# Kernel tuning notes

Measured on AMD Instinct MI355X. Metric: run time of the kernel, lower is better.

Reference implementation:

```python
import jax, jax.numpy as jnp
import numpy as np

C0 = 0.5 * np.sqrt(1.0 / np.pi)
C1 = np.sqrt(3.0 / (4 * np.pi))
C2 = 0.5 * np.sqrt(15.0 / (4 * np.pi))
C20 = 0.5 * np.sqrt(5.0 / (16 * np.pi))
C22 = 0.5 * np.sqrt(15.0 / (16 * np.pi))


def sh_basis(d):
    # d: [N,3] unit directions -> [N,9] (degree 2, matches torch code order)
    x, y, z = d[:, 0], d[:, 1], d[:, 2]
    return jnp.stack([
        C0 * jnp.ones_like(x),
        C1 * y, C1 * z, C1 * x,
        C2 * x * y, C2 * y * z,
        C20 * (3 * z * z - 1),
        C2 * x * z,
        C22 * (x * x - y * y),
    ], axis=-1)


def trilinear_sample(voxels, pts_norm):
    # voxels: [R,R,R,F] indexed (z,y,x); pts_norm: [N,3] in [-1,1] (x,y,z)
    # Matches F.grid_sample(align_corners=True, padding_mode='border').
    R = voxels.shape[0]
    c = jnp.clip((pts_norm + 1.0) * 0.5 * (R - 1), 0.0, R - 1)  # border clamp
    c0 = jnp.floor(c)
    f = c - c0                          # [N,3] fractional weights (fx,fy,fz)
    i0 = c0.astype(jnp.int32)
    i1 = jnp.minimum(i0 + 1, R - 1)
    x0, y0, z0 = i0[:, 0], i0[:, 1], i0[:, 2]
    x1, y1, z1 = i1[:, 0], i1[:, 1], i1[:, 2]
    fx, fy, fz = f[:, 0:1], f[:, 1:2], f[:, 2:3]
    g = lambda zi, yi, xi: voxels[zi, yi, xi]  # gather -> [N,F]
    c00 = g(z0, y0, x0) * (1 - fx) + g(z0, y0, x1) * fx
    c01 = g(z0, y1, x0) * (1 - fx) + g(z0, y1, x1) * fx
    c10 = g(z1, y0, x0) * (1 - fx) + g(z1, y0, x1) * fx
    c11 = g(z1, y1, x0) * (1 - fx) + g(z1, y1, x1) * fx
    c0_ = c00 * (1 - fy) + c01 * fy
    c1_ = c10 * (1 - fy) + c11 * fy
    return c0_ * (1 - fz) + c1_ * fz


def setup_inputs() -> dict:
    key = jax.random.key(0)
    k1, k2 = jax.random.split(key)
    N, R, F = 2_000_000, 192, 28
    points = jax.random.normal(k1, (N, 3), dtype=jnp.float32)
    voxels = jax.random.normal(k2, (R, R, R, F), dtype=jnp.float32) * 0.1
    return {"points": points, "voxels": voxels}


def reference(points, voxels):
    N = points.shape[0]
    sh_dim = 9
    pts_norm = points / 4.0
    feats = trilinear_sample(voxels, pts_norm)         # [N, 28]
    density = feats[:, 0]
    sh = feats[:, 1:].reshape(N, 3, sh_dim)            # [N,3,9]
    d = points / jnp.linalg.norm(points, axis=-1, keepdims=True)
    basis = sh_basis(d)[:, None, :]                    # [N,1,9]
    rgb = jax.nn.sigmoid(jnp.sum(sh * basis, axis=-1))  # [N,3]
    sigma = jax.nn.softplus(density)[:, None]           # [N,1]
    return rgb, sigma
```

## Files before the change

### kernel.cpp

```cpp
#include <hip/hip_runtime.h>
#include <math.h>

#define RDIM 192
#define FDIM 28
#define PTS_PER_BLOCK 32

#define SH_C0  0.28209479177387814f
#define SH_C1  0.4886025119029199f
#define SH_C2  0.5462742152960396f
#define SH_C20 0.15769578262626154f
#define SH_C22 0.2731371076480198f

__global__ __launch_bounds__(256)
void plenoxel_fwd(const float* __restrict__ points,
                  const float* __restrict__ voxels,
                  float* __restrict__ out_rgb,
                  float* __restrict__ out_sigma,
                  int N)
{
    __shared__ float feats[PTS_PER_BLOCK][FDIM];

    const int tid   = threadIdx.x;
    const int group = tid >> 3;
    const int f     = tid & 7;
    const int p     = blockIdx.x * PTS_PER_BLOCK + group;

    if (p < N && f < 7) {
        float px = points[3 * p + 0];
        float py = points[3 * p + 1];
        float pz = points[3 * p + 2];

        const float A = (RDIM - 1) / 8.0f;
        const float B = (RDIM - 1) * 0.5f;
        const float RM1 = (float)(RDIM - 1);
        float cx = fminf(fmaxf(px * A + B, 0.0f), RM1);
        float cy = fminf(fmaxf(py * A + B, 0.0f), RM1);
        float cz = fminf(fmaxf(pz * A + B, 0.0f), RM1);

        float cx0 = floorf(cx), cy0 = floorf(cy), cz0 = floorf(cz);
        float fx = cx - cx0, fy = cy - cy0, fz = cz - cz0;
        int x0 = (int)cx0, y0 = (int)cy0, z0 = (int)cz0;
        int x1 = min(x0 + 1, RDIM - 1);
        int y1 = min(y0 + 1, RDIM - 1);
        int z1 = min(z0 + 1, RDIM - 1);

        float gx = 1.0f - fx, gy = 1.0f - fy, gz = 1.0f - fz;

        float w000 = gz * gy * gx;
        float w001 = gz * gy * fx;
        float w010 = gz * fy * gx;
        float w011 = gz * fy * fx;
        float w100 = fz * gy * gx;
        float w101 = fz * gy * fx;
        float w110 = fz * fy * gx;
        float w111 = fz * fy * fx;

        int b000 = ((z0 * RDIM + y0) * RDIM + x0) * FDIM;
        int b001 = ((z0 * RDIM + y0) * RDIM + x1) * FDIM;
        int b010 = ((z0 * RDIM + y1) * RDIM + x0) * FDIM;
        int b011 = ((z0 * RDIM + y1) * RDIM + x1) * FDIM;
        int b100 = ((z1 * RDIM + y0) * RDIM + x0) * FDIM;
        int b101 = ((z1 * RDIM + y0) * RDIM + x1) * FDIM;
        int b110 = ((z1 * RDIM + y1) * RDIM + x0) * FDIM;
        int b111 = ((z1 * RDIM + y1) * RDIM + x1) * FDIM;

        const float4* __restrict__ src = (const float4*)voxels;

        float4 v0 = src[(b000 >> 2) + f];
        float4 v1 = src[(b001 >> 2) + f];
        float4 v2 = src[(b010 >> 2) + f];
        float4 v3 = src[(b011 >> 2) + f];
        float4 v4 = src[(b100 >> 2) + f];
        float4 v5 = src[(b101 >> 2) + f];
        float4 v6 = src[(b110 >> 2) + f];
        float4 v7 = src[(b111 >> 2) + f];

        float4 acc;
        acc.x = w000 * v0.x + w001 * v1.x + w010 * v2.x + w011 * v3.x
              + w100 * v4.x + w101 * v5.x + w110 * v6.x + w111 * v7.x;
        acc.y = w000 * v0.y + w001 * v1.y + w010 * v2.y + w011 * v3.y
              + w100 * v4.y + w101 * v5.y + w110 * v6.y + w111 * v7.y;
        acc.z = w000 * v0.z + w001 * v1.z + w010 * v2.z + w011 * v3.z
              + w100 * v4.z + w101 * v5.z + w110 * v6.z + w111 * v7.z;
        acc.w = w000 * v0.w + w001 * v1.w + w010 * v2.w + w011 * v3.w
              + w100 * v4.w + w101 * v5.w + w110 * v6.w + w111 * v7.w;

        *(float4*)&feats[group][4 * f] = acc;
    }

    __syncthreads();

    if (tid < PTS_PER_BLOCK) {
        int p2 = blockIdx.x * PTS_PER_BLOCK + tid;
        if (p2 < N) {
            float px = points[3 * p2 + 0];
            float py = points[3 * p2 + 1];
            float pz = points[3 * p2 + 2];

            float inv = rsqrtf(px * px + py * py + pz * pz);
            float dx = px * inv, dy = py * inv, dz = pz * inv;

            float basis[9];
            basis[0] = SH_C0;
            basis[1] = SH_C1 * dy;
            basis[2] = SH_C1 * dz;
            basis[3] = SH_C1 * dx;
            basis[4] = SH_C2 * dx * dy;
            basis[5] = SH_C2 * dy * dz;
            basis[6] = SH_C20 * (3.0f * dz * dz - 1.0f);
            basis[7] = SH_C2 * dx * dz;
            basis[8] = SH_C22 * (dx * dx - dy * dy);

#pragma unroll
            for (int c = 0; c < 3; ++c) {
                float s = 0.0f;
#pragma unroll
                for (int j = 0; j < 9; ++j) {
                    s += feats[tid][1 + 9 * c + j] * basis[j];
                }
                out_rgb[3 * p2 + c] = 1.0f / (1.0f + expf(-s));
            }

            float x = feats[tid][0];
            out_sigma[p2] = fmaxf(x, 0.0f) + log1pf(expf(-fabsf(x)));
        }
    }
}

extern "C" void kernel_launch(void* const* d_in, const int* in_sizes, int n_in,
                              void* d_out, int out_size, void* d_ws, size_t ws_size,
                              hipStream_t stream) {
    const float* points = (const float*)d_in[0];
    const float* voxels = (const float*)d_in[1];
    int N = in_sizes[0] / 3;

    float* out_rgb = (float*)d_out;
    float* out_sigma = out_rgb + (size_t)3 * N;

    int blocks = (N + PTS_PER_BLOCK - 1) / PTS_PER_BLOCK;
    plenoxel_fwd<<<blocks, 256, 0, stream>>>(points, voxels, out_rgb, out_sigma, N);
}
```

Baseline: 354.3 us.

## Bucket-sort points by voxel block before trilinear gather for locality

```diff
diff --git a/kernel.cpp b/kernel.cpp
--- a/kernel.cpp
+++ b/kernel.cpp
@@ -4,6 +4,10 @@
 #define RDIM 192
 #define FDIM 28
 #define PTS_PER_BLOCK 32
+
+#define BSHIFT 3
+#define BDIM   (RDIM >> BSHIFT)
+#define NBUCKET (BDIM * BDIM * BDIM)
 
 #define SH_C0  0.28209479177387814f
 #define SH_C1  0.4886025119029199f
@@ -11,8 +15,89 @@
 #define SH_C20 0.15769578262626154f
 #define SH_C22 0.2731371076480198f
 
-__global__ __launch_bounds__(256)
-void plenoxel_fwd(const float* __restrict__ points,
+__device__ __forceinline__ void cell_of(float px, float py, float pz,
+                                        int& x0, int& y0, int& z0) {
+    const float A = (RDIM - 1) / 8.0f;
+    const float B = (RDIM - 1) * 0.5f;
+    const float RM1 = (float)(RDIM - 1);
+    float cx = fminf(fmaxf(px * A + B, 0.0f), RM1);
+    float cy = fminf(fmaxf(py * A + B, 0.0f), RM1);
+    float cz = fminf(fmaxf(pz * A + B, 0.0f), RM1);
+    x0 = (int)floorf(cx);
+    y0 = (int)floorf(cy);
+    z0 = (int)floorf(cz);
+}
+
+__device__ __forceinline__ int bucket_of(int x0, int y0, int z0) {
+    return ((z0 >> BSHIFT) * BDIM + (y0 >> BSHIFT)) * BDIM + (x0 >> BSHIFT);
+}
+
+__global__ __launch_bounds__(256)
+void zero_hist(int* __restrict__ hist) {
+    int i = blockIdx.x * 256 + threadIdx.x;
+    if (i < NBUCKET) hist[i] = 0;
+}
+
+__global__ __launch_bounds__(256)
+void hist_kernel(const float* __restrict__ points, int* __restrict__ hist, int N) {
+    int i = blockIdx.x * 256 + threadIdx.x;
+    if (i >= N) return;
+    float px = points[3 * i + 0];
+    float py = points[3 * i + 1];
+    float pz = points[3 * i + 2];
+    int x0, y0, z0;
+    cell_of(px, py, pz, x0, y0, z0);
+    atomicAdd(&hist[bucket_of(x0, y0, z0)], 1);
+}
+
+#define SCAN_T 1024
+#define SCAN_V 14
+__global__ __launch_bounds__(SCAN_T)
+void scan_kernel(const int* __restrict__ hist, int* __restrict__ offs) {
+    __shared__ int lds[SCAN_T];
+    int t = threadIdx.x;
+    int base = t * SCAN_V;
+    int v[SCAN_V];
+    int s = 0;
+#pragma unroll
+    for (int k = 0; k < SCAN_V; ++k) {
+        int idx = base + k;
+        v[k] = (idx < NBUCKET) ? hist[idx] : 0;
+        s += v[k];
+    }
+    lds[t] = s;
+    __syncthreads();
+    for (int off = 1; off < SCAN_T; off <<= 1) {
+        int add = (t >= off) ? lds[t - off] : 0;
+        __syncthreads();
+        lds[t] += add;
+        __syncthreads();
+    }
+    int excl = (t == 0) ? 0 : lds[t - 1];
+#pragma unroll
+    for (int k = 0; k < SCAN_V; ++k) {
+        int idx = base + k;
+        if (idx < NBUCKET) offs[idx] = excl;
+        excl += v[k];
+    }
+}
+
+__global__ __launch_bounds__(256)
+void scatter_kernel(const float* __restrict__ points, int* __restrict__ offs,
+                    float4* __restrict__ sorted, int N) {
+    int i = blockIdx.x * 256 + threadIdx.x;
+    if (i >= N) return;
+    float px = points[3 * i + 0];
+    float py = points[3 * i + 1];
+    float pz = points[3 * i + 2];
+    int x0, y0, z0;
+    cell_of(px, py, pz, x0, y0, z0);
+    int pos = atomicAdd(&offs[bucket_of(x0, y0, z0)], 1);
+    sorted[pos] = make_float4(px, py, pz, __int_as_float(i));
+}
+
+__global__ __launch_bounds__(256)
+void plenoxel_fwd(const float4* __restrict__ sorted,
                   const float* __restrict__ voxels,
                   float* __restrict__ out_rgb,
                   float* __restrict__ out_sigma,
@@ -26,20 +111,18 @@
     const int p     = blockIdx.x * PTS_PER_BLOCK + group;
 
     if (p < N && f < 7) {
-        float px = points[3 * p + 0];
-        float py = points[3 * p + 1];
-        float pz = points[3 * p + 2];
-
+        float4 pt = sorted[p];
+        float px = pt.x, py = pt.y, pz = pt.z;
+
+        int x0, y0, z0;
+        cell_of(px, py, pz, x0, y0, z0);
         const float A = (RDIM - 1) / 8.0f;
         const float B = (RDIM - 1) * 0.5f;
         const float RM1 = (float)(RDIM - 1);
         float cx = fminf(fmaxf(px * A + B, 0.0f), RM1);
         float cy = fminf(fmaxf(py * A + B, 0.0f), RM1);
         float cz = fminf(fmaxf(pz * A + B, 0.0f), RM1);
-
-        float cx0 = floorf(cx), cy0 = floorf(cy), cz0 = floorf(cz);
-        float fx = cx - cx0, fy = cy - cy0, fz = cz - cz0;
-        int x0 = (int)cx0, y0 = (int)cy0, z0 = (int)cz0;
+        float fx = cx - (float)x0, fy = cy - (float)y0, fz = cz - (float)z0;
         int x1 = min(x0 + 1, RDIM - 1);
         int y1 = min(y0 + 1, RDIM - 1);
         int z1 = min(z0 + 1, RDIM - 1);
@@ -93,9 +176,9 @@
     if (tid < PTS_PER_BLOCK) {
         int p2 = blockIdx.x * PTS_PER_BLOCK + tid;
         if (p2 < N) {
-            float px = points[3 * p2 + 0];
-            float py = points[3 * p2 + 1];
-            float pz = points[3 * p2 + 2];
+            float4 pt = sorted[p2];
+            float px = pt.x, py = pt.y, pz = pt.z;
+            int oi = __float_as_int(pt.w);
 
             float inv = rsqrtf(px * px + py * py + pz * pz);
             float dx = px * inv, dy = py * inv, dz = pz * inv;
@@ -118,11 +201,11 @@
                 for (int j = 0; j < 9; ++j) {
                     s += feats[tid][1 + 9 * c + j] * basis[j];
                 }
-                out_rgb[3 * p2 + c] = 1.0f / (1.0f + expf(-s));
+                out_rgb[3 * oi + c] = 1.0f / (1.0f + expf(-s));
             }
 
             float x = feats[tid][0];
-            out_sigma[p2] = fmaxf(x, 0.0f) + log1pf(expf(-fabsf(x)));
+            out_sigma[oi] = fmaxf(x, 0.0f) + log1pf(expf(-fabsf(x)));
         }
     }
 }
@@ -137,6 +220,18 @@
     float* out_rgb = (float*)d_out;
     float* out_sigma = out_rgb + (size_t)3 * N;
 
-    int blocks = (N + PTS_PER_BLOCK - 1) / PTS_PER_BLOCK;
-    plenoxel_fwd<<<blocks, 256, 0, stream>>>(points, voxels, out_rgb, out_sigma, N);
-}
+    char* ws = (char*)d_ws;
+    float4* sorted = (float4*)ws;
+    int* hist = (int*)(ws + (size_t)N * 16);
+    int* offs = hist + NBUCKET;
+
+    int pblocks = (N + 255) / 256;
+
+    zero_hist<<<(NBUCKET + 255) / 256, 256, 0, stream>>>(hist);
+    hist_kernel<<<pblocks, 256, 0, stream>>>(points, hist, N);
+    scan_kernel<<<1, SCAN_T, 0, stream>>>(hist, offs);
+    scatter_kernel<<<pblocks, 256, 0, stream>>>(points, offs, sorted, N);
+
+    int gblocks = (N + PTS_PER_BLOCK - 1) / PTS_PER_BLOCK;
+    plenoxel_fwd<<<gblocks, 256, 0, stream>>>(sorted, voxels, out_rgb, out_sigma, N);
+}
```

Result: slower. 823.3 us (+132.3%).

## Process two points per thread group to double in-flight gathers

Applied to the files above, without the earlier changes.

```diff
diff --git a/kernel.cpp b/kernel.cpp
--- a/kernel.cpp
+++ b/kernel.cpp
@@ -3,7 +3,7 @@
 
 #define RDIM 192
 #define FDIM 28
-#define PTS_PER_BLOCK 32
+#define PPB 64
 
 #define SH_C0  0.28209479177387814f
 #define SH_C1  0.4886025119029199f
@@ -18,84 +18,101 @@
                   float* __restrict__ out_sigma,
                   int N)
 {
-    __shared__ float feats[PTS_PER_BLOCK][FDIM];
+    __shared__ float feats[PPB][FDIM];
+    __shared__ float4 plds[PPB];
 
     const int tid   = threadIdx.x;
     const int group = tid >> 3;
     const int f     = tid & 7;
-    const int p     = blockIdx.x * PTS_PER_BLOCK + group;
+    const int pbase = blockIdx.x * PPB;
+    const float4* __restrict__ src = (const float4*)voxels;
 
-    if (p < N && f < 7) {
-        float px = points[3 * p + 0];
-        float py = points[3 * p + 1];
-        float pz = points[3 * p + 2];
+    const float A   = (RDIM - 1) / 8.0f;
+    const float B   = (RDIM - 1) * 0.5f;
+    const float RM1 = (float)(RDIM - 1);
 
-        const float A = (RDIM - 1) / 8.0f;
-        const float B = (RDIM - 1) * 0.5f;
-        const float RM1 = (float)(RDIM - 1);
-        float cx = fminf(fmaxf(px * A + B, 0.0f), RM1);
-        float cy = fminf(fmaxf(py * A + B, 0.0f), RM1);
-        float cz = fminf(fmaxf(pz * A + B, 0.0f), RM1);
+    if (f < 7) {
+#define POINT_SETUP(h, PIDX)                                                  \
+        const int p##h  = (PIDX);                                             \
+        const int cp##h = min(p##h, N - 1);                                   \
+        const float px##h = points[3 * cp##h + 0];                            \
+        const float py##h = points[3 * cp##h + 1];                            \
+        const float pz##h = points[3 * cp##h + 2];                            \
+        if (f == 0) plds[group + 32 * h] =                                    \
+            make_float4(px##h, py##h, pz##h, 0.0f);                           \
+        float cx##h = fminf(fmaxf(px##h * A + B, 0.0f), RM1);                 \
+        float cy##h = fminf(fmaxf(py##h * A + B, 0.0f), RM1);                 \
+        float cz##h = fminf(fmaxf(pz##h * A + B, 0.0f), RM1);                 \
+        float fcx##h = floorf(cx##h), fcy##h = floorf(cy##h),                 \
+              fcz##h = floorf(cz##h);                                         \
+        float fx##h = cx##h - fcx##h, fy##h = cy##h - fcy##h,                 \
+              fz##h = cz##h - fcz##h;                                         \
+        int x0##h = (int)fcx##h, y0##h = (int)fcy##h, z0##h = (int)fcz##h;    \
+        int x1##h = min(x0##h + 1, RDIM - 1);                                 \
+        int y1##h = min(y0##h + 1, RDIM - 1);                                 \
+        int z1##h = min(z0##h + 1, RDIM - 1);                                 \
+        float gx##h = 1.0f - fx##h, gy##h = 1.0f - fy##h,                     \
+              gz##h = 1.0f - fz##h;                                           \
+        float w##h##0 = gz##h * gy##h * gx##h;                                \
+        float w##h##1 = gz##h * gy##h * fx##h;                                \
+        float w##h##2 = gz##h * fy##h * gx##h;                                \
+        float w##h##3 = gz##h * fy##h * fx##h;                                \
+        float w##h##4 = fz##h * gy##h * gx##h;                                \
+        float w##h##5 = fz##h * gy##h * fx##h;                                \
+        float w##h##6 = fz##h * fy##h * gx##h;                                \
+        float w##h##7 = fz##h * fy##h * fx##h;                                \
+        int a##h##0 = ((((z0##h * RDIM + y0##h) * RDIM + x0##h) * FDIM) >> 2) + f; \
+        int a##h##1 = ((((z0##h * RDIM + y0##h) * RDIM + x1##h) * FDIM) >> 2) + f; \
+        int a##h##2 = ((((z0##h * RDIM + y1##h) * RDIM + x0##h) * FDIM) >> 2) + f; \
+        int a##h##3 = ((((z0##h * RDIM + y1##h) * RDIM + x1##h) * FDIM) >> 2) + f; \
+        int a##h##4 = ((((z1##h * RDIM + y0##h) * RDIM + x0##h) * FDIM) >> 2) + f; \
+        int a##h##5 = ((((z1##h * RDIM + y0##h) * RDIM + x1##h) * FDIM) >> 2) + f; \
+        int a##h##6 = ((((z1##h * RDIM + y1##h) * RDIM + x0##h) * FDIM) >> 2) + f; \
+        int a##h##7 = ((((z1##h * RDIM + y1##h) * RDIM + x1##h) * FDIM) >> 2) + f;
 
-        float cx0 = floorf(cx), cy0 = floorf(cy), cz0 = floorf(cz);
-        float fx = cx - cx0, fy = cy - cy0, fz = cz - cz0;
-        int x0 = (int)cx0, y0 = (int)cy0, z0 = (int)cz0;
-        int x1 = min(x0 + 1, RDIM - 1);
-        int y1 = min(y0 + 1, RDIM - 1);
-        int z1 = min(z0 + 1, RDIM - 1);
+        POINT_SETUP(0, pbase + group)
+        POINT_SETUP(1, pbase + group + 32)
+#undef POINT_SETUP
 
-        float gx = 1.0f - fx, gy = 1.0f - fy, gz = 1.0f - fz;
+        float4 v00 = src[a00]; float4 v01 = src[a01];
+        float4 v02 = src[a02]; float4 v03 = src[a03];
+        float4 v04 = src[a04]; float4 v05 = src[a05];
+        float4 v06 = src[a06]; float4 v07 = src[a07];
+        float4 v10 = src[a10]; float4 v11 = src[a11];
+        float4 v12 = src[a12]; float4 v13 = src[a13];
+        float4 v14 = src[a14]; float4 v15 = src[a15];
+        float4 v16 = src[a16]; float4 v17 = src[a17];
 
-        float w000 = gz * gy * gx;
-        float w001 = gz * gy * fx;
-        float w010 = gz * fy * gx;
-        float w011 = gz * fy * fx;
-        float w100 = fz * gy * gx;
-        float w101 = fz * gy * fx;
-        float w110 = fz * fy * gx;
-        float w111 = fz * fy * fx;
+#define ACC_STORE(h, V0, V1, V2, V3, V4, V5, V6, V7, ROW)                     \
+        {                                                                     \
+            float4 acc;                                                       \
+            acc.x = w##h##0 * V0.x + w##h##1 * V1.x + w##h##2 * V2.x          \
+                  + w##h##3 * V3.x + w##h##4 * V4.x + w##h##5 * V5.x          \
+                  + w##h##6 * V6.x + w##h##7 * V7.x;                          \
+            acc.y = w##h##0 * V0.y + w##h##1 * V1.y + w##h##2 * V2.y          \
+                  + w##h##3 * V3.y + w##h##4 * V4.y + w##h##5 * V5.y          \
+                  + w##h##6 * V6.y + w##h##7 * V7.y;                          \
+            acc.z = w##h##0 * V0.z + w##h##1 * V1.z + w##h##2 * V2.z          \
+                  + w##h##3 * V3.z + w##h##4 * V4.z + w##h##5 * V5.z          \
+                  + w##h##6 * V6.z + w##h##7 * V7.z;                          \
+            acc.w = w##h##0 * V0.w + w##h##1 * V1.w + w##h##2 * V2.w          \
+                  + w##h##3 * V3.w + w##h##4 * V4.w + w##h##5 * V5.w          \
+                  + w##h##6 * V6.w + w##h##7 * V7.w;                          \
+            *(float4*)&feats[ROW][4 * f] = acc;                               \
+        }
 
-        int b000 = ((z0 * RDIM + y0) * RDIM + x0) * FDIM;
-        int b001 = ((z0 * RDIM + y0) * RDIM + x1) * FDIM;
-        int b010 = ((z0 * RDIM + y1) * RDIM + x0) * FDIM;
-        int b011 = ((z0 * RDIM + y1) * RDIM + x1) * FDIM;
-        int b100 = ((z1 * RDIM + y0) * RDIM + x0) * FDIM;
-        int b101 = ((z1 * RDIM + y0) * RDIM + x1) * FDIM;
-        int b110 = ((z1 * RDIM + y1) * RDIM + x0) * FDIM;
-        int b111 = ((z1 * RDIM + y1) * RDIM + x1) * FDIM;
-
-        const float4* __restrict__ src = (const float4*)voxels;
-
-        float4 v0 = src[(b000 >> 2) + f];
-        float4 v1 = src[(b001 >> 2) + f];
-        float4 v2 = src[(b010 >> 2) + f];
-        float4 v3 = src[(b011 >> 2) + f];
-        float4 v4 = src[(b100 >> 2) + f];
-        float4 v5 = src[(b101 >> 2) + f];
-        float4 v6 = src[(b110 >> 2) + f];
-        float4 v7 = src[(b111 >> 2) + f];
-
-        float4 acc;
-        acc.x = w000 * v0.x + w001 * v1.x + w010 * v2.x + w011 * v3.x
-              + w100 * v4.x + w101 * v5.x + w110 * v6.x + w111 * v7.x;
-        acc.y = w000 * v0.y + w001 * v1.y + w010 * v2.y + w011 * v3.y
-              + w100 * v4.y + w101 * v5.y + w110 * v6.y + w111 * v7.y;
-        acc.z = w000 * v0.z + w001 * v1.z + w010 * v2.z + w011 * v3.z
-              + w100 * v4.z + w101 * v5.z + w110 * v6.z + w111 * v7.z;
-        acc.w = w000 * v0.w + w001 * v1.w + w010 * v2.w + w011 * v3.w
-              + w100 * v4.w + w101 * v5.w + w110 * v6.w + w111 * v7.w;
-
-        *(float4*)&feats[group][4 * f] = acc;
+        ACC_STORE(0, v00, v01, v02, v03, v04, v05, v06, v07, group)
+        ACC_STORE(1, v10, v11, v12, v13, v14, v15, v16, v17, group + 32)
+#undef ACC_STORE
     }
 
     __syncthreads();
 
-    if (tid < PTS_PER_BLOCK) {
-        int p2 = blockIdx.x * PTS_PER_BLOCK + tid;
+    if (tid < PPB) {
+        int p2 = pbase + tid;
         if (p2 < N) {
-            float px = points[3 * p2 + 0];
-            float py = points[3 * p2 + 1];
-            float pz = points[3 * p2 + 2];
+            float4 pt = plds[tid];
+            float px = pt.x, py = pt.y, pz = pt.z;
 
             float inv = rsqrtf(px * px + py * py + pz * pz);
             float dx = px * inv, dy = py * inv, dz = pz * inv;
@@ -118,11 +135,13 @@
                 for (int j = 0; j < 9; ++j) {
                     s += feats[tid][1 + 9 * c + j] * basis[j];
                 }
-                out_rgb[3 * p2 + c] = 1.0f / (1.0f + expf(-s));
+                float r = 1.0f / (1.0f + expf(-s));
+                __builtin_nontemporal_store(r, &out_rgb[3 * p2 + c]);
             }
 
             float x = feats[tid][0];
-            out_sigma[p2] = fmaxf(x, 0.0f) + log1pf(expf(-fabsf(x)));
+            float sig = fmaxf(x, 0.0f) + log1pf(expf(-fabsf(x)));
+            __builtin_nontemporal_store(sig, &out_sigma[p2]);
         }
     }
 }
@@ -137,6 +156,6 @@
     float* out_rgb = (float*)d_out;
     float* out_sigma = out_rgb + (size_t)3 * N;
 
-    int blocks = (N + PTS_PER_BLOCK - 1) / PTS_PER_BLOCK;
+    int blocks = (N + PPB - 1) / PPB;
     plenoxel_fwd<<<blocks, 256, 0, stream>>>(points, voxels, out_rgb, out_sigma, N);
 }
```

New measurement: 350.5 us. No clear change (-1.1%).
